# Optimization experiments

Measured on AMD Instinct MI355X. Metric: run time of the kernel, lower is better.

The kernel has to match this reference:

```python
import jax, jax.numpy as jnp
import numpy as np

N = 20000          # nodes
E = 320000         # edges
H = 128            # hidden_channels
A = 512            # aerial feature dim
SPOT = 20000
DIST_UNIT = 50
NEMB = SPOT // DIST_UNIT
RATIO = 0.25       # neighbor_ratio


def setup_inputs() -> dict:
    key = jax.random.key(0)
    ks = jax.random.split(key, 12)
    x = jax.random.normal(ks[0], (N, H), jnp.float32)
    edge_index = jax.random.randint(ks[1], (2, E), 0, N)
    distances = jax.random.randint(ks[2], (E,), 0, SPOT)
    aerial_emb = jax.random.normal(ks[3], (N, A), jnp.float32)
    s = lambda k, shape, fan: jax.random.normal(k, shape, jnp.float32) / np.sqrt(fan).astype(np.float32)
    W_lin = s(ks[4], (H, H), H)
    b_lin = jnp.zeros((H,), jnp.float32)
    W_q = s(ks[5], (H + A + H, H), H + A + H)
    b_q = jnp.zeros((H,), jnp.float32)
    W_v = s(ks[6], (H, H), H)
    b_v = jnp.zeros((H,), jnp.float32)
    dist_table = jax.random.normal(ks[7], (NEMB, H), jnp.float32)  # init.normal_ like torch
    W_l = s(ks[8], (H, H), H)   # SAGE lin_l (neighbor aggr), with bias
    b_l = jnp.zeros((H,), jnp.float32)
    W_r = s(ks[9], (H, H), H)   # SAGE lin_r (root), no bias in PyG default
    return dict(x=x, edge_index=edge_index, distances=distances, aerial_emb=aerial_emb,
                W_lin=W_lin, b_lin=b_lin, W_q=W_q, b_q=b_q, W_v=W_v, b_v=b_v,
                dist_table=dist_table, W_l=W_l, b_l=b_l, W_r=W_r)


def reference(x, edge_index, distances, aerial_emb, W_lin, b_lin, W_q, b_q, W_v, b_v, dist_table, W_l, b_l, W_r):
    n = x.shape[0]
    e = edge_index.shape[1]
    k = int(e * RATIO)  # static: number of sampled edges

    x = x @ W_lin + b_lin                                  # [N, H]
    src, tgt = edge_index[0], edge_index[1]
    source_x = x[src]                                      # [E, H]
    target_x = x[tgt]                                      # [E, H]
    source_aerial = aerial_emb[src]                        # [E, A]
    dist_x = dist_table[distances // DIST_UNIT]            # [E, H]

    query = jnp.concatenate([source_x, source_aerial, dist_x], axis=1) @ W_q + b_q  # [E, H]
    value = target_x @ W_v + b_v                           # [E, H]
    logits = -jnp.linalg.norm(query - value, axis=1)       # [E]
    logprob = jax.nn.log_softmax(logits, axis=0)

    # torch.multinomial(prob, k) without replacement == Gumbel top-k on log-probs
    u = jax.random.uniform(jax.random.key(42), (e,), jnp.float32)
    gumbel = -jnp.log(-jnp.log(u + 1e-20) + 1e-20)
    _, sel = jax.lax.top_k(logprob + gumbel, k)            # [k] selected edge ids
    src_s = src[sel]
    tgt_s = tgt[sel]

    # SAGEConv (mean aggregation): out = lin_l(mean_j x_j) + lin_r(x)
    msg = jax.ops.segment_sum(x[src_s], tgt_s, num_segments=n)              # [N, H]
    deg = jax.ops.segment_sum(jnp.ones((k,), x.dtype), tgt_s, num_segments=n)
    aggr = msg / jnp.maximum(deg, 1.0)[:, None]
    out = aggr @ W_l + b_l + x @ W_r                       # [N, H]
    return out
```

## Files before the change

kernel.cpp:

```cpp
#include <hip/hip_runtime.h>
#include <stdint.h>

#define N_NODES 20000
#define E_EDGES 320000
#define H_DIM 128
#define A_DIM 512
#define NEMB_N 400
#define K_SEL 80000u
#define NB1 16384
#define NB2 16384
#define CAND_MAX 8192
#define LO_F (-128.0f)
#define SCALE1 (16384.0f / 160.0f)
#define KN_M 32

struct SelState {
    int b1; unsigned cum1; unsigned r1;
    int b2; unsigned cum2; unsigned r2;
    unsigned long long T;
};

__device__ __forceinline__ uint32_t rotl32(uint32_t x, int r) {
    return (x << r) | (x >> (32 - r));
}

__device__ __forceinline__ void threefry2x32(uint32_t k0, uint32_t k1,
                                             uint32_t& x0, uint32_t& x1) {
    uint32_t ks0 = k0, ks1 = k1, ks2 = k0 ^ k1 ^ 0x1BD11BDAu;
    x0 += ks0; x1 += ks1;
    x0 += x1; x1 = rotl32(x1, 13); x1 ^= x0;
    x0 += x1; x1 = rotl32(x1, 15); x1 ^= x0;
    x0 += x1; x1 = rotl32(x1, 26); x1 ^= x0;
    x0 += x1; x1 = rotl32(x1, 6);  x1 ^= x0;
    x0 += ks1; x1 += ks2 + 1u;
    x0 += x1; x1 = rotl32(x1, 17); x1 ^= x0;
    x0 += x1; x1 = rotl32(x1, 29); x1 ^= x0;
    x0 += x1; x1 = rotl32(x1, 16); x1 ^= x0;
    x0 += x1; x1 = rotl32(x1, 24); x1 ^= x0;
    x0 += ks2; x1 += ks0 + 2u;
    x0 += x1; x1 = rotl32(x1, 13); x1 ^= x0;
    x0 += x1; x1 = rotl32(x1, 15); x1 ^= x0;
    x0 += x1; x1 = rotl32(x1, 26); x1 ^= x0;
    x0 += x1; x1 = rotl32(x1, 6);  x1 ^= x0;
    x0 += ks0; x1 += ks1 + 3u;
    x0 += x1; x1 = rotl32(x1, 17); x1 ^= x0;
    x0 += x1; x1 = rotl32(x1, 29); x1 ^= x0;
    x0 += x1; x1 = rotl32(x1, 16); x1 ^= x0;
    x0 += x1; x1 = rotl32(x1, 24); x1 ^= x0;
    x0 += ks1; x1 += ks2 + 4u;
    x0 += x1; x1 = rotl32(x1, 13); x1 ^= x0;
    x0 += x1; x1 = rotl32(x1, 15); x1 ^= x0;
    x0 += x1; x1 = rotl32(x1, 26); x1 ^= x0;
    x0 += x1; x1 = rotl32(x1, 6);  x1 ^= x0;
    x0 += ks2; x1 += ks0 + 5u;
}

__global__ __launch_bounds__(256) void k_node(
    const float* __restrict__ x, const float* __restrict__ aerial,
    const float* __restrict__ Wlin, const float* __restrict__ blin,
    const float* __restrict__ Wq, const float* __restrict__ bq,
    const float* __restrict__ Wv, const float* __restrict__ bv,
    float* __restrict__ xl32, float* __restrict__ q32, float* __restrict__ v32) {
    __shared__ float bufA[H_DIM][KN_M + 4];
    __shared__ float bufX[H_DIM][KN_M + 4];
    const int tid = threadIdx.x;
    const int g   = tid >> 5;
    const int jj  = tid & 31;
    const int nb  = g * 4;
    const int n0  = blockIdx.x * KN_M;
    const int c0 = jj, c1 = jj + 32, c2 = jj + 64, c3 = jj + 96;
    const int dd = tid & 127;
    const int nh = (tid >> 7) * 16;

    for (int m = 0; m < 16; ++m)
        bufA[dd][nh + m] = x[(size_t)(n0 + nh + m) * H_DIM + dd];
    __syncthreads();

    float accL[4][4];
    {
        float b0 = blin[c0], b1 = blin[c1], b2 = blin[c2], b3 = blin[c3];
#pragma unroll
        for (int i = 0; i < 4; ++i) {
            accL[0][i] = b0; accL[1][i] = b1; accL[2][i] = b2; accL[3][i] = b3;
        }
    }
#pragma unroll 4
    for (int k = 0; k < H_DIM; ++k) {
        const float4 xa = *(const float4*)&bufA[k][nb];
        const float w0 = Wlin[k * H_DIM + c0];
        const float w1 = Wlin[k * H_DIM + c1];
        const float w2 = Wlin[k * H_DIM + c2];
        const float w3 = Wlin[k * H_DIM + c3];
        const float xv[4] = {xa.x, xa.y, xa.z, xa.w};
#pragma unroll
        for (int i = 0; i < 4; ++i) {
            accL[0][i] = fmaf(xv[i], w0, accL[0][i]);
            accL[1][i] = fmaf(xv[i], w1, accL[1][i]);
            accL[2][i] = fmaf(xv[i], w2, accL[2][i]);
            accL[3][i] = fmaf(xv[i], w3, accL[3][i]);
        }
    }
#pragma unroll
    for (int c = 0; c < 4; ++c) {
        const int col = jj + c * 32;
#pragma unroll
        for (int i = 0; i < 4; ++i) {
            xl32[(size_t)(n0 + nb + i) * H_DIM + col] = accL[c][i];
            bufX[col][nb + i] = accL[c][i];
        }
    }
    __syncthreads();

    float accV[4][4], accQ[4][4];
    {
        float v0 = bv[c0], v1 = bv[c1], v2 = bv[c2], v3 = bv[c3];
        float q0 = bq[c0], q1 = bq[c1], q2 = bq[c2], q3 = bq[c3];
#pragma unroll
        for (int i = 0; i < 4; ++i) {
            accV[0][i] = v0; accV[1][i] = v1; accV[2][i] = v2; accV[3][i] = v3;
            accQ[0][i] = q0; accQ[1][i] = q1; accQ[2][i] = q2; accQ[3][i] = q3;
        }
    }
#pragma unroll 4
    for (int k = 0; k < H_DIM; ++k) {
        const float4 xa = *(const float4*)&bufX[k][nb];
        const float wv0 = Wv[k * H_DIM + c0];
        const float wv1 = Wv[k * H_DIM + c1];
        const float wv2 = Wv[k * H_DIM + c2];
        const float wv3 = Wv[k * H_DIM + c3];
        const float wq0 = Wq[k * H_DIM + c0];
        const float wq1 = Wq[k * H_DIM + c1];
        const float wq2 = Wq[k * H_DIM + c2];
        const float wq3 = Wq[k * H_DIM + c3];
        const float xv[4] = {xa.x, xa.y, xa.z, xa.w};
#pragma unroll
        for (int i = 0; i < 4; ++i) {
            accV[0][i] = fmaf(xv[i], wv0, accV[0][i]);
            accV[1][i] = fmaf(xv[i], wv1, accV[1][i]);
            accV[2][i] = fmaf(xv[i], wv2, accV[2][i]);
            accV[3][i] = fmaf(xv[i], wv3, accV[3][i]);
            accQ[0][i] = fmaf(xv[i], wq0, accQ[0][i]);
            accQ[1][i] = fmaf(xv[i], wq1, accQ[1][i]);
            accQ[2][i] = fmaf(xv[i], wq2, accQ[2][i]);
            accQ[3][i] = fmaf(xv[i], wq3, accQ[3][i]);
        }
    }
#pragma unroll
    for (int c = 0; c < 4; ++c) {
        const int col = jj + c * 32;
#pragma unroll
        for (int i = 0; i < 4; ++i)
            v32[(size_t)(n0 + nb + i) * H_DIM + col] = accV[c][i];
    }

    for (int ch = 0; ch < 4; ++ch) {
        __syncthreads();
        for (int m = 0; m < 16; ++m)
            bufA[dd][nh + m] = aerial[(size_t)(n0 + nh + m) * A_DIM + ch * H_DIM + dd];
        __syncthreads();
        const float* Wqc = Wq + (size_t)(H_DIM + ch * H_DIM) * H_DIM;
#pragma unroll 4
        for (int k = 0; k < H_DIM; ++k) {
            const float4 xa = *(const float4*)&bufA[k][nb];
            const float w0 = Wqc[k * H_DIM + c0];
            const float w1 = Wqc[k * H_DIM + c1];
            const float w2 = Wqc[k * H_DIM + c2];
            const float w3 = Wqc[k * H_DIM + c3];
            const float xv[4] = {xa.x, xa.y, xa.z, xa.w};
#pragma unroll
            for (int i = 0; i < 4; ++i) {
                accQ[0][i] = fmaf(xv[i], w0, accQ[0][i]);
                accQ[1][i] = fmaf(xv[i], w1, accQ[1][i]);
                accQ[2][i] = fmaf(xv[i], w2, accQ[2][i]);
                accQ[3][i] = fmaf(xv[i], w3, accQ[3][i]);
            }
        }
    }
#pragma unroll
    for (int c = 0; c < 4; ++c) {
        const int col = jj + c * 32;
#pragma unroll
        for (int i = 0; i < 4; ++i)
            q32[(size_t)(n0 + nb + i) * H_DIM + col] = accQ[c][i];
    }
}

__global__ __launch_bounds__(128) void k_dist(
    const float* __restrict__ dtab, const float* __restrict__ Wq,
    float* __restrict__ dq32) {
    __shared__ float dsT[H_DIM][8];
    const int j = threadIdx.x;
    const int n0 = blockIdx.x * 8;
#pragma unroll
    for (int m = 0; m < 8; ++m) dsT[j][m] = dtab[(size_t)(n0 + m) * H_DIM + j];
    __syncthreads();
    float acc[8];
#pragma unroll
    for (int m = 0; m < 8; ++m) acc[m] = 0.0f;
    for (int k = 0; k < H_DIM; ++k) {
        float w = Wq[(size_t)(H_DIM + A_DIM + k) * H_DIM + j];
        const float4* xp = (const float4*)&dsT[k][0];
        float4 a0 = xp[0], a1 = xp[1];
        acc[0] = fmaf(a0.x, w, acc[0]); acc[1] = fmaf(a0.y, w, acc[1]);
        acc[2] = fmaf(a0.z, w, acc[2]); acc[3] = fmaf(a0.w, w, acc[3]);
        acc[4] = fmaf(a1.x, w, acc[4]); acc[5] = fmaf(a1.y, w, acc[5]);
        acc[6] = fmaf(a1.z, w, acc[6]); acc[7] = fmaf(a1.w, w, acc[7]);
    }
#pragma unroll
    for (int m = 0; m < 8; ++m) dq32[(size_t)(n0 + m) * H_DIM + j] = acc[m];
}

__device__ __forceinline__ int bin1_of(float s) {
    float t = (s - LO_F) * SCALE1;
    int b = (int)t;
    return min(max(b, 0), NB1 - 1);
}
__device__ __forceinline__ int bin2_of(float s, int b1) {
    float t = (s - LO_F) * SCALE1;
    float frac = t - (float)b1;
    int b = (int)(frac * (float)NB2);
    return min(max(b, 0), NB2 - 1);
}

__global__ __launch_bounds__(256) void k_score(
    const int* __restrict__ ei, const int* __restrict__ dist,
    const float* __restrict__ q32, const float* __restrict__ v32,
    const float* __restrict__ dq32,
    unsigned long long* __restrict__ keys, float* __restrict__ s32o) {
    const int half = threadIdx.x >> 5, lane = threadIdx.x & 31;
    const int e0 = blockIdx.x * 32 + half * 4;
    int sidx[4], tidx[4], db[4];
#pragma unroll
    for (int i = 0; i < 4; ++i) {
        sidx[i] = ei[e0 + i];
        tidx[i] = ei[E_EDGES + e0 + i];
        db[i] = dist[e0 + i] / 50;
    }
    float4 q[4], v[4], d[4];
#pragma unroll
    for (int i = 0; i < 4; ++i)
        q[i] = ((const float4*)(q32 + (size_t)sidx[i] * H_DIM))[lane];
#pragma unroll
    for (int i = 0; i < 4; ++i)
        v[i] = ((const float4*)(v32 + (size_t)tidx[i] * H_DIM))[lane];
#pragma unroll
    for (int i = 0; i < 4; ++i)
        d[i] = ((const float4*)(dq32 + (size_t)db[i] * H_DIM))[lane];
    uint32_t r0 = 0u, r1 = (uint32_t)(e0 + (lane & 3));
    threefry2x32(0u, 42u, r0, r1);
    uint32_t fb = ((r0 ^ r1) >> 9) | 0x3f800000u;
    float uu_l = __uint_as_float(fb) - 1.0f;

    float ss[4];
#pragma unroll
    for (int i = 0; i < 4; ++i) {
        float dx = q[i].x + d[i].x - v[i].x;
        float dy = q[i].y + d[i].y - v[i].y;
        float dz = q[i].z + d[i].z - v[i].z;
        float dw = q[i].w + d[i].w - v[i].w;
        float t = fmaf(dx, dx, fmaf(dy, dy, fmaf(dz, dz, dw * dw)));
#pragma unroll
        for (int o = 16; o > 0; o >>= 1) t += __shfl_xor(t, o, 64);
        ss[i] = t;
    }
    if (lane < 4) {
        float myss = ss[0];
        if (lane == 1) myss = ss[1];
        if (lane == 2) myss = ss[2];
        if (lane == 3) myss = ss[3];
        float nrm = sqrtf(myss);
        float a = -logf(uu_l + 1e-20f);
        float g = -logf(a + 1e-20f);
        float score = g - nrm;
        int ib = __float_as_int(score);
        unsigned m32 = (ib < 0) ? ~(unsigned)ib : ((unsigned)ib | 0x80000000u);
        const int e = e0 + lane;
        keys[e] = ((unsigned long long)m32 << 32) |
                  (unsigned)(0xFFFFFFFFu - (unsigned)e);
        s32o[e] = score;
    }
}

__global__ __launch_bounds__(256) void k_hist1(const float* __restrict__ s32,
                                               unsigned* __restrict__ hist1) {
    int e = blockIdx.x * 256 + threadIdx.x;
    atomicAdd(&hist1[bin1_of(s32[e])], 1u);
}

__global__ __launch_bounds__(256) void k_hist2(const float* __restrict__ s32,
                                               const SelState* __restrict__ st,
                                               unsigned* __restrict__ hist2) {
    int e = blockIdx.x * 256 + threadIdx.x;
    float s = s32[e];
    int b1 = bin1_of(s);
    if (b1 != st->b1) return;
    atomicAdd(&hist2[bin2_of(s, b1)], 1u);
}

__global__ __launch_bounds__(256) void k_scan(const unsigned* __restrict__ hist,
                                              SelState* st, int phase) {
    __shared__ unsigned csum[256];
    __shared__ unsigned bins[64];
    __shared__ int selc;
    __shared__ unsigned cumbase;
    const int t = threadIdx.x;
    const unsigned target = (phase == 1) ? K_SEL : st->r1;
    unsigned s = 0;
    for (int i = 0; i < 64; ++i) s += hist[t * 64 + i];
    csum[t] = s;
    __syncthreads();
    if (t == 0) {
        unsigned cum = 0; int c = 255;
        for (; c >= 0; --c) {
            if (cum + csum[c] >= target) break;
            cum += csum[c];
        }
        selc = c; cumbase = cum;
    }
    __syncthreads();
    if (t < 64) bins[t] = hist[selc * 64 + t];
    __syncthreads();
    if (t == 0) {
        unsigned cum = cumbase; int b = -1;
        for (int i = 63; i >= 0; --i) {
            if (cum + bins[i] >= target) { b = selc * 64 + i; break; }
            cum += bins[i];
        }
        unsigned r = target - cum;
        if (phase == 1) { st->b1 = b; st->cum1 = cum; st->r1 = r; }
        else           { st->b2 = b; st->cum2 = cum; st->r2 = r; }
    }
}

__global__ __launch_bounds__(256) void k_collect(
    const float* __restrict__ s32, const unsigned long long* __restrict__ keys,
    const SelState* __restrict__ st, unsigned long long* __restrict__ cand,
    unsigned* __restrict__ cnt) {
    int e = blockIdx.x * 256 + threadIdx.x;
    float s = s32[e];
    int b1 = bin1_of(s);
    if (b1 != st->b1) return;
    if (bin2_of(s, b1) != st->b2) return;
    unsigned p = atomicAdd(cnt, 1u);
    if (p < CAND_MAX) cand[p] = keys[e];
}

__global__ __launch_bounds__(256) void k_thresh(
    const unsigned long long* __restrict__ cand, const unsigned* __restrict__ cnt,
    SelState* st) {
    int c = (int)min(*cnt, (unsigned)CAND_MAX);
    unsigned r2 = st->r2;
    for (int i = threadIdx.x; i < c; i += blockDim.x) {
        unsigned long long ki = cand[i];
        unsigned g = 0;
        for (int j = 0; j < c; ++j) g += (cand[j] > ki);
        if (g == r2 - 1) st->T = ki;
    }
}

__global__ __launch_bounds__(256) void k_scatter(
    const int* __restrict__ ei, const unsigned long long* __restrict__ keys,
    const SelState* __restrict__ st, const float* __restrict__ xl32,
    float* __restrict__ msg, float* __restrict__ deg) {
    const int wid = threadIdx.x >> 6, lane = threadIdx.x & 63;
    const int e = blockIdx.x * 4 + wid;
    if (keys[e] >= st->T) {
        int sidx = ei[e], tidx = ei[E_EDGES + e];
        const float* xp = xl32 + (size_t)sidx * H_DIM;
        float* mp = msg + (size_t)tidx * H_DIM;
        const int h = lane * 2;
        atomicAdd(&mp[h], xp[h]);
        atomicAdd(&mp[h + 1], xp[h + 1]);
        if (lane == 0) atomicAdd(&deg[tidx], 1.0f);
    }
}

__global__ __launch_bounds__(128) void k_out(
    const float* __restrict__ msg, const float* __restrict__ deg,
    const float* __restrict__ xl32, const float* __restrict__ Wl,
    const float* __restrict__ bl, const float* __restrict__ Wr,
    float* __restrict__ out) {
    __shared__ float axT[H_DIM][8];
    __shared__ float xxT[H_DIM][8];
    const int j = threadIdx.x;
    const int n0 = blockIdx.x * 8;
#pragma unroll
    for (int m = 0; m < 8; ++m) {
        float d = fmaxf(deg[n0 + m], 1.0f);
        axT[j][m] = msg[(size_t)(n0 + m) * H_DIM + j] / d;
        xxT[j][m] = xl32[(size_t)(n0 + m) * H_DIM + j];
    }
    __syncthreads();
    float acc[8];
    float bj = bl[j];
#pragma unroll
    for (int m = 0; m < 8; ++m) acc[m] = bj;
    for (int k = 0; k < H_DIM; ++k) {
        float wl = Wl[k * H_DIM + j];
        float wr = Wr[k * H_DIM + j];
        const float4* ap = (const float4*)&axT[k][0];
        const float4* xp = (const float4*)&xxT[k][0];
        float4 a0 = ap[0], a1 = ap[1];
        float4 x0 = xp[0], x1 = xp[1];
        acc[0] = fmaf(a0.x, wl, fmaf(x0.x, wr, acc[0]));
        acc[1] = fmaf(a0.y, wl, fmaf(x0.y, wr, acc[1]));
        acc[2] = fmaf(a0.z, wl, fmaf(x0.z, wr, acc[2]));
        acc[3] = fmaf(a0.w, wl, fmaf(x0.w, wr, acc[3]));
        acc[4] = fmaf(a1.x, wl, fmaf(x1.x, wr, acc[4]));
        acc[5] = fmaf(a1.y, wl, fmaf(x1.y, wr, acc[5]));
        acc[6] = fmaf(a1.z, wl, fmaf(x1.z, wr, acc[6]));
        acc[7] = fmaf(a1.w, wl, fmaf(x1.w, wr, acc[7]));
    }
#pragma unroll
    for (int m = 0; m < 8; ++m) out[(size_t)(n0 + m) * H_DIM + j] = acc[m];
}

extern "C" void kernel_launch(void* const* d_in, const int* in_sizes, int n_in,
                              void* d_out, int out_size, void* d_ws, size_t ws_size,
                              hipStream_t stream) {
    const float* x      = (const float*)d_in[0];
    const int*   ei     = (const int*)d_in[1];
    const int*   dist   = (const int*)d_in[2];
    const float* aerial = (const float*)d_in[3];
    const float* Wlin   = (const float*)d_in[4];
    const float* blin   = (const float*)d_in[5];
    const float* Wq     = (const float*)d_in[6];
    const float* bq     = (const float*)d_in[7];
    const float* Wv     = (const float*)d_in[8];
    const float* bv     = (const float*)d_in[9];
    const float* dtab   = (const float*)d_in[10];
    const float* Wl     = (const float*)d_in[11];
    const float* bl     = (const float*)d_in[12];
    const float* Wr     = (const float*)d_in[13];
    float* out = (float*)d_out;

    char* ws = (char*)d_ws;
    size_t off = 0;
    auto alloc = [&](size_t bytes) -> void* {
        void* p = ws + off;
        off += (bytes + 255) & ~(size_t)255;
        return p;
    };
    float* q32  = (float*)alloc((size_t)N_NODES * H_DIM * 4);
    float* v32  = (float*)alloc((size_t)N_NODES * H_DIM * 4);
    float* dq32 = (float*)alloc((size_t)NEMB_N * H_DIM * 4);
    unsigned long long* keys = (unsigned long long*)alloc((size_t)E_EDGES * 8);
    float* xl32 = (float*)alloc((size_t)N_NODES * H_DIM * 4);
    float* s32  = (float*)alloc((size_t)E_EDGES * 4);
    char* zbase = ws + off;
    float* msg  = (float*)alloc((size_t)N_NODES * H_DIM * 4);
    float* deg  = (float*)alloc((size_t)N_NODES * 4);
    unsigned* hist1 = (unsigned*)alloc((size_t)NB1 * 4);
    unsigned* hist2 = (unsigned*)alloc((size_t)NB2 * 4);
    unsigned long long* cand = (unsigned long long*)alloc((size_t)CAND_MAX * 8);
    unsigned* counters = (unsigned*)alloc(256);
    SelState* st = (SelState*)alloc(256);
    size_t zlen = (size_t)((ws + off) - zbase);

    hipMemsetAsync(zbase, 0, zlen, stream);

    k_node<<<N_NODES / KN_M, 256, 0, stream>>>(x, aerial, Wlin, blin, Wq, bq, Wv, bv,
                                               xl32, q32, v32);
    k_dist<<<NEMB_N / 8, 128, 0, stream>>>(dtab, Wq, dq32);
    k_score<<<E_EDGES / 32, 256, 0, stream>>>(ei, dist, q32, v32, dq32, keys, s32);
    k_hist1<<<E_EDGES / 256, 256, 0, stream>>>(s32, hist1);
    k_scan<<<1, 256, 0, stream>>>(hist1, st, 1);
    k_hist2<<<E_EDGES / 256, 256, 0, stream>>>(s32, st, hist2);
    k_scan<<<1, 256, 0, stream>>>(hist2, st, 2);
    k_collect<<<E_EDGES / 256, 256, 0, stream>>>(s32, keys, st, cand, &counters[0]);
    k_thresh<<<1, 256, 0, stream>>>(cand, &counters[0], st);
    k_scatter<<<E_EDGES / 4, 256, 0, stream>>>(ei, keys, st, xl32, msg, deg);
    k_out<<<N_NODES / 8, 128, 0, stream>>>(msg, deg, xl32, Wl, bl, Wr, out);
}
```

Baseline: 517.3 us.

## Retile node projection kernel: 64 nodes per block, wave-uniform weight columns

Rewrites the per-node projection kernel so each block handles 64 nodes and each wavefront owns a contiguous 32-column slice. The column index is made wave-uniform with readfirstlane, so weight rows can be fetched as scalar/broadcast loads, while each lane holds one node with 32 accumulators. The V and Q projections are split into separate passes, and xl32 is written back with coalesced float4 stores via shared memory. The aim is to cut per-lane weight load traffic and improve weight reuse, at the cost of higher register pressure, a partial last block and extra bounds handling.

```diff
diff --git a/kernel.cpp b/kernel.cpp
--- a/kernel.cpp
+++ b/kernel.cpp
@@ -12,7 +12,7 @@
 #define CAND_MAX 8192
 #define LO_F (-128.0f)
 #define SCALE1 (16384.0f / 160.0f)
-#define KN_M 32
+#define KN_T 64
 
 struct SelState {
     int b1; unsigned cum1; unsigned r1;
@@ -61,127 +61,100 @@
     const float* __restrict__ Wq, const float* __restrict__ bq,
     const float* __restrict__ Wv, const float* __restrict__ bv,
     float* __restrict__ xl32, float* __restrict__ q32, float* __restrict__ v32) {
-    __shared__ float bufA[H_DIM][KN_M + 4];
-    __shared__ float bufX[H_DIM][KN_M + 4];
+    __shared__ float bufA[H_DIM][KN_T + 1];
+    __shared__ float bufX[H_DIM][KN_T + 1];
     const int tid = threadIdx.x;
-    const int g   = tid >> 5;
-    const int jj  = tid & 31;
-    const int nb  = g * 4;
-    const int n0  = blockIdx.x * KN_M;
-    const int c0 = jj, c1 = jj + 32, c2 = jj + 64, c3 = jj + 96;
-    const int dd = tid & 127;
-    const int nh = (tid >> 7) * 16;
-
-    for (int m = 0; m < 16; ++m)
-        bufA[dd][nh + m] = x[(size_t)(n0 + nh + m) * H_DIM + dd];
-    __syncthreads();
-
-    float accL[4][4];
+    const int n   = tid & 63;
+    const int wv  = __builtin_amdgcn_readfirstlane(tid >> 6);
+    const int cb  = wv * 32;
+    const int n0  = blockIdx.x * KN_T;
+    const int d   = tid & 127;
+    const int hh  = (tid >> 7) * 32;
+    const bool wr = (n0 + n) < N_NODES;
+
+    for (int m = 0; m < 32; ++m) {
+        int node = min(n0 + hh + m, N_NODES - 1);
+        bufA[d][hh + m] = x[(size_t)node * H_DIM + d];
+    }
+    __syncthreads();
+
+    float accL[32];
+#pragma unroll
+    for (int c = 0; c < 32; ++c) accL[c] = blin[cb + c];
+#pragma unroll 2
+    for (int k = 0; k < H_DIM; ++k) {
+        float xk = bufA[k][n];
+        const float* Wr = Wlin + (size_t)k * H_DIM + cb;
+#pragma unroll
+        for (int c = 0; c < 32; ++c) accL[c] = fmaf(xk, Wr[c], accL[c]);
+    }
+#pragma unroll
+    for (int c = 0; c < 32; ++c) bufX[cb + c][n] = accL[c];
+    __syncthreads();
+
     {
-        float b0 = blin[c0], b1 = blin[c1], b2 = blin[c2], b3 = blin[c3];
-#pragma unroll
-        for (int i = 0; i < 4; ++i) {
-            accL[0][i] = b0; accL[1][i] = b1; accL[2][i] = b2; accL[3][i] = b3;
+        const int nn  = tid >> 2;
+        const int cb2 = (tid & 3) * 32;
+        if (n0 + nn < N_NODES) {
+#pragma unroll
+            for (int cc = 0; cc < 32; cc += 4) {
+                float4 t;
+                t.x = bufX[cb2 + cc + 0][nn];
+                t.y = bufX[cb2 + cc + 1][nn];
+                t.z = bufX[cb2 + cc + 2][nn];
+                t.w = bufX[cb2 + cc + 3][nn];
+                *(float4*)&xl32[(size_t)(n0 + nn) * H_DIM + cb2 + cc] = t;
+            }
         }
     }
-#pragma unroll 4
+
+    float accV[32];
+#pragma unroll
+    for (int c = 0; c < 32; ++c) accV[c] = bv[cb + c];
+#pragma unroll 2
     for (int k = 0; k < H_DIM; ++k) {
-        const float4 xa = *(const float4*)&bufA[k][nb];
-        const float w0 = Wlin[k * H_DIM + c0];
-        const float w1 = Wlin[k * H_DIM + c1];
-        const float w2 = Wlin[k * H_DIM + c2];
-        const float w3 = Wlin[k * H_DIM + c3];
-        const float xv[4] = {xa.x, xa.y, xa.z, xa.w};
-#pragma unroll
-        for (int i = 0; i < 4; ++i) {
-            accL[0][i] = fmaf(xv[i], w0, accL[0][i]);
-            accL[1][i] = fmaf(xv[i], w1, accL[1][i]);
-            accL[2][i] = fmaf(xv[i], w2, accL[2][i]);
-            accL[3][i] = fmaf(xv[i], w3, accL[3][i]);
+        float xk = bufX[k][n];
+        const float* Wr = Wv + (size_t)k * H_DIM + cb;
+#pragma unroll
+        for (int c = 0; c < 32; ++c) accV[c] = fmaf(xk, Wr[c], accV[c]);
+    }
+    if (wr) {
+#pragma unroll
+        for (int c = 0; c < 32; ++c)
+            v32[(size_t)(n0 + n) * H_DIM + cb + c] = accV[c];
+    }
+
+    float accQ[32];
+#pragma unroll
+    for (int c = 0; c < 32; ++c) accQ[c] = bq[cb + c];
+#pragma unroll 2
+    for (int k = 0; k < H_DIM; ++k) {
+        float xk = bufX[k][n];
+        const float* Wr = Wq + (size_t)k * H_DIM + cb;
+#pragma unroll
+        for (int c = 0; c < 32; ++c) accQ[c] = fmaf(xk, Wr[c], accQ[c]);
+    }
+
+    for (int ch = 0; ch < 4; ++ch) {
+        if (ch > 0) __syncthreads();
+        for (int m = 0; m < 32; ++m) {
+            int node = min(n0 + hh + m, N_NODES - 1);
+            bufA[d][hh + m] = aerial[(size_t)node * A_DIM + ch * H_DIM + d];
         }
-    }
-#pragma unroll
-    for (int c = 0; c < 4; ++c) {
-        const int col = jj + c * 32;
-#pragma unroll
-        for (int i = 0; i < 4; ++i) {
-            xl32[(size_t)(n0 + nb + i) * H_DIM + col] = accL[c][i];
-            bufX[col][nb + i] = accL[c][i];
-        }
-    }
-    __syncthreads();
-
-    float accV[4][4], accQ[4][4];
-    {
-        float v0 = bv[c0], v1 = bv[c1], v2 = bv[c2], v3 = bv[c3];
-        float q0 = bq[c0], q1 = bq[c1], q2 = bq[c2], q3 = bq[c3];
-#pragma unroll
-        for (int i = 0; i < 4; ++i) {
-            accV[0][i] = v0; accV[1][i] = v1; accV[2][i] = v2; accV[3][i] = v3;
-            accQ[0][i] = q0; accQ[1][i] = q1; accQ[2][i] = q2; accQ[3][i] = q3;
-        }
-    }
-#pragma unroll 4
-    for (int k = 0; k < H_DIM; ++k) {
-        const float4 xa = *(const float4*)&bufX[k][nb];
-        const float wv0 = Wv[k * H_DIM + c0];
-        const float wv1 = Wv[k * H_DIM + c1];
-        const float wv2 = Wv[k * H_DIM + c2];
-        const float wv3 = Wv[k * H_DIM + c3];
-        const float wq0 = Wq[k * H_DIM + c0];
-        const float wq1 = Wq[k * H_DIM + c1];
-        const float wq2 = Wq[k * H_DIM + c2];
-        const float wq3 = Wq[k * H_DIM + c3];
-        const float xv[4] = {xa.x, xa.y, xa.z, xa.w};
-#pragma unroll
-        for (int i = 0; i < 4; ++i) {
-            accV[0][i] = fmaf(xv[i], wv0, accV[0][i]);
-            accV[1][i] = fmaf(xv[i], wv1, accV[1][i]);
-            accV[2][i] = fmaf(xv[i], wv2, accV[2][i]);
-            accV[3][i] = fmaf(xv[i], wv3, accV[3][i]);
-            accQ[0][i] = fmaf(xv[i], wq0, accQ[0][i]);
-            accQ[1][i] = fmaf(xv[i], wq1, accQ[1][i]);
-            accQ[2][i] = fmaf(xv[i], wq2, accQ[2][i]);
-            accQ[3][i] = fmaf(xv[i], wq3, accQ[3][i]);
-        }
-    }
-#pragma unroll
-    for (int c = 0; c < 4; ++c) {
-        const int col = jj + c * 32;
-#pragma unroll
-        for (int i = 0; i < 4; ++i)
-            v32[(size_t)(n0 + nb + i) * H_DIM + col] = accV[c][i];
-    }
-
-    for (int ch = 0; ch < 4; ++ch) {
-        __syncthreads();
-        for (int m = 0; m < 16; ++m)
-            bufA[dd][nh + m] = aerial[(size_t)(n0 + nh + m) * A_DIM + ch * H_DIM + dd];
         __syncthreads();
         const float* Wqc = Wq + (size_t)(H_DIM + ch * H_DIM) * H_DIM;
-#pragma unroll 4
+#pragma unroll 2
         for (int k = 0; k < H_DIM; ++k) {
-            const float4 xa = *(const float4*)&bufA[k][nb];
-            const float w0 = Wqc[k * H_DIM + c0];
-            const float w1 = Wqc[k * H_DIM + c1];
-            const float w2 = Wqc[k * H_DIM + c2];
-            const float w3 = Wqc[k * H_DIM + c3];
-            const float xv[4] = {xa.x, xa.y, xa.z, xa.w};
-#pragma unroll
-            for (int i = 0; i < 4; ++i) {
-                accQ[0][i] = fmaf(xv[i], w0, accQ[0][i]);
-                accQ[1][i] = fmaf(xv[i], w1, accQ[1][i]);
-                accQ[2][i] = fmaf(xv[i], w2, accQ[2][i]);
-                accQ[3][i] = fmaf(xv[i], w3, accQ[3][i]);
-            }
+            float xk = bufA[k][n];
+            const float* Wr = Wqc + (size_t)k * H_DIM + cb;
+#pragma unroll
+            for (int c = 0; c < 32; ++c) accQ[c] = fmaf(xk, Wr[c], accQ[c]);
         }
     }
-#pragma unroll
-    for (int c = 0; c < 4; ++c) {
-        const int col = jj + c * 32;
-#pragma unroll
-        for (int i = 0; i < 4; ++i)
-            q32[(size_t)(n0 + nb + i) * H_DIM + col] = accQ[c][i];
+    if (wr) {
+#pragma unroll
+        for (int c = 0; c < 32; ++c)
+            q32[(size_t)(n0 + n) * H_DIM + cb + c] = accQ[c];
     }
 }
 
@@ -459,8 +432,8 @@
 
     hipMemsetAsync(zbase, 0, zlen, stream);
 
-    k_node<<<N_NODES / KN_M, 256, 0, stream>>>(x, aerial, Wlin, blin, Wq, bq, Wv, bv,
-                                               xl32, q32, v32);
+    k_node<<<(N_NODES + KN_T - 1) / KN_T, 256, 0, stream>>>(
+        x, aerial, Wlin, blin, Wq, bq, Wv, bv, xl32, q32, v32);
     k_dist<<<NEMB_N / 8, 128, 0, stream>>>(dtab, Wq, dq32);
     k_score<<<E_EDGES / 32, 256, 0, stream>>>(ei, dist, q32, v32, dq32, keys, s32);
     k_hist1<<<E_EDGES / 256, 256, 0, stream>>>(s32, hist1);
```

Result: slower. 561.5 us (+8.5%).
